# Kernel optimization log

Measured on AMD Instinct MI355X. Metric: run time of the kernel, lower is better.

Reference implementation:

```python
import jax, jax.numpy as jnp
import numpy as np

N_NODES = 50000
N_EDGES = 625000
DIM = 128
DROPOUT_P = 0.5


def setup_inputs() -> dict:
    key = jax.random.key(0)
    kx, ke, kw, kb = jax.random.split(key, 4)
    x = jax.random.normal(kx, (N_NODES, DIM), dtype=jnp.float32)
    edge_index = jax.random.randint(ke, (2, N_EDGES), 0, N_NODES, dtype=jnp.int64)
    # GCNConv linear weight (glorot-ish) and bias
    W = jax.random.normal(kw, (DIM, DIM), dtype=jnp.float32) / np.sqrt(DIM)
    b = jnp.zeros((DIM,), dtype=jnp.float32)
    return {"x": x, "edge_index": edge_index, "W": W, "b": b}


def reference(x, edge_index, W, b):
    N = x.shape[0]
    # --- add self-loops ---
    loop = jnp.arange(N, dtype=edge_index.dtype)
    src = jnp.concatenate([edge_index[0], loop])  # [E+N]
    dst = jnp.concatenate([edge_index[1], loop])  # [E+N]
    # --- symmetric normalization: deg computed on destination nodes ---
    deg = jax.ops.segment_sum(jnp.ones_like(src, dtype=x.dtype), dst, num_segments=N)
    dis = jnp.where(deg > 0, jax.lax.rsqrt(jnp.where(deg > 0, deg, 1.0)), 0.0)
    norm = dis[src] * dis[dst]  # [E+N]
    # --- linear transform, gather, scatter-add ---
    h = x @ W  # [N, D]
    msg = h[src] * norm[:, None]  # [E+N, D]
    out = jax.ops.segment_sum(msg, dst, num_segments=N) + b  # [N, D]
    # --- ReLU + dropout (training mode, fixed key) + residual ---
    out = jax.nn.relu(out)
    keep = jax.random.bernoulli(jax.random.key(42), 1.0 - DROPOUT_P, out.shape)
    out = jnp.where(keep, out / (1.0 - DROPOUT_P), 0.0)
    out = out + x  # residual: input_dim == output_dim
    return out
```

## Files before the change

kernel.cpp:

```cpp
#include <hip/hip_runtime.h>
#include <hip/hip_bf16.h>
#include <stdint.h>

#define NDIM 128
#define LDK 136
#define BSH 9
#define NB_A 1024
#define BCAP 9216

typedef __attribute__((ext_vector_type(8))) short bf16x8;
typedef __attribute__((ext_vector_type(4))) float f32x4;

__device__ __forceinline__ unsigned short f2bf(float f) {
    unsigned u = __float_as_uint(f);
    unsigned r = u + 0x7fffu + ((u >> 16) & 1u);
    return (unsigned short)(r >> 16);
}
__device__ __forceinline__ float bf2f(unsigned short s) {
    return __uint_as_float(((unsigned)s) << 16);
}

__device__ __forceinline__ void load_edge(const unsigned* __restrict__ w, int is64, int E,
                                          int e, int& s, int& d) {
    if (is64) {
        s = (int)w[(size_t)2 * e];
        d = (int)w[(size_t)2 * E + (size_t)2 * e];
    } else {
        s = (int)w[e];
        d = (int)w[(size_t)E + e];
    }
}

__device__ __forceinline__ int detect_is64(const unsigned* __restrict__ w,
                                           int lo, int hi, int t, int* nzflag) {
    if (t == 0) *nzflag = 0;
    __syncthreads();
    int k = lo + t;
    if (k < hi && w[2 * (size_t)k + 1] != 0u) atomicOr(nzflag, 1);
    __syncthreads();
    return *nzflag ? 0 : 1;
}

__global__ __launch_bounds__(256) void hist_kernel(const unsigned* __restrict__ w,
                                                   const float* __restrict__ W,
                                                   unsigned short* __restrict__ WbfT,
                                                   int* __restrict__ hist,
                                                   int* __restrict__ lock,
                                                   int E, int nbuck, int chunk) {
    __shared__ int h[128];
    __shared__ int nzflag;
    int t = threadIdx.x;
    if (t < 128) h[t] = 0;
    if (t == 0 && blockIdx.x == 0) *lock = 0;
    int lo = blockIdx.x * chunk;
    int hi = lo + chunk; if (hi > E) hi = E;
    int is64 = detect_is64(w, lo, hi, t, &nzflag);

    if (blockIdx.x < 64) {
        int idx = blockIdx.x * 256 + t;
        int k = idx >> 7, c = idx & 127;
        WbfT[c * 128 + k] = f2bf(W[idx]);
    }

    for (int e = lo + t; e < hi; e += 256) {
        int s, d; load_edge(w, is64, E, e, s, d);
        atomicAdd(&h[d >> BSH], 1);
    }
    __syncthreads();
    if (t < nbuck) hist[(size_t)t * gridDim.x + blockIdx.x] = h[t];
}

__global__ __launch_bounds__(1024) void scanhist_kernel(int* __restrict__ hist,
                                                        int* __restrict__ btot,
                                                        int* __restrict__ bbase,
                                                        int* __restrict__ off,
                                                        int* __restrict__ lock,
                                                        int NB, int nbuck, int N, int E) {
    __shared__ int s[1024];
    __shared__ int amlast;
    int t = threadIdx.x;
    if (t == 0) amlast = 0;
    size_t base = (size_t)blockIdx.x * NB;
    int v = hist[base + t];
    s[t] = v;
    __syncthreads();
    for (int d = 1; d < 1024; d <<= 1) {
        int add = (t >= d) ? s[t - d] : 0;
        __syncthreads();
        s[t] += add;
        __syncthreads();
    }
    hist[base + t] = s[t] - v;
    if (t == 1023) {
        atomicExch(&btot[blockIdx.x], s[1023]);
        __threadfence();
        int prev = atomicAdd(lock, 1);
        amlast = (prev == nbuck - 1) ? 1 : 0;
    }
    __syncthreads();
    if (amlast) {
        int v2 = (t < nbuck) ? atomicAdd(&btot[t], 0) : 0;
        s[t] = v2;
        __syncthreads();
        for (int d = 1; d < 128; d <<= 1) {
            int add = (t >= d && t < 128) ? s[t - d] : 0;
            __syncthreads();
            if (t < 128) s[t] += add;
            __syncthreads();
        }
        if (t < nbuck) bbase[t] = s[t] - v2;
        if (t == 0) off[N] = E;
    }
}

__global__ __launch_bounds__(256) void bucket_kernel(const unsigned* __restrict__ w,
                                                     const int* __restrict__ hist,
                                                     const int* __restrict__ bbase,
                                                     unsigned* __restrict__ ebuf,
                                                     int E, int nbuck, int chunk) {
    __shared__ int cur[128];
    __shared__ int nzflag;
    int t = threadIdx.x;
    if (t < nbuck) cur[t] = bbase[t] + hist[(size_t)t * gridDim.x + blockIdx.x];
    int lo = blockIdx.x * chunk;
    int hi = lo + chunk; if (hi > E) hi = E;
    int is64 = detect_is64(w, lo, hi, t, &nzflag);
    for (int e = lo + t; e < hi; e += 256) {
        int s, d; load_edge(w, is64, E, e, s, d);
        int b = d >> BSH;
        int p = atomicAdd(&cur[b], 1);
        ebuf[p] = ((unsigned)s << BSH) | (unsigned)(d & 511);
    }
}

__global__ __launch_bounds__(512) void csrgemm_kernel(const unsigned* __restrict__ ebuf,
                                                      const int* __restrict__ bbase,
                                                      const int* __restrict__ btot,
                                                      int* __restrict__ adj,
                                                      int* __restrict__ off,
                                                      float* __restrict__ dis,
                                                      const float* __restrict__ x,
                                                      const unsigned short* __restrict__ WbfT,
                                                      unsigned short* __restrict__ hp,
                                                      int N, int nbuck) {
    __shared__ union {
        struct { int lcnt[512]; int lscan[512]; int cur[512]; int tile[BCAP]; } cs;
        unsigned short Wt[NDIM][LDK];
    } u;
    int t = threadIdx.x;
    if (blockIdx.x < nbuck) {
        int b = blockIdx.x;
        int start = bbase[b], cnt = btot[b];
        u.cs.lcnt[t] = 0;
        __syncthreads();
        for (int i = t; i < cnt; i += 512) atomicAdd(&u.cs.lcnt[ebuf[start + i] & 511], 1);
        __syncthreads();
        int v = u.cs.lcnt[t];
        u.cs.lscan[t] = v;
        __syncthreads();
        for (int d = 1; d < 512; d <<= 1) {
            int add = (t >= d) ? u.cs.lscan[t - d] : 0;
            __syncthreads();
            u.cs.lscan[t] += add;
            __syncthreads();
        }
        int ex = u.cs.lscan[t] - v;
        int node = (b << BSH) + t;
        if (node < N) {
            off[node] = start + ex;
            dis[node] = rsqrtf((float)(v + 1));
        }
        u.cs.cur[t] = ex;
        __syncthreads();
        if (cnt <= BCAP) {
            for (int i = t; i < cnt; i += 512) {
                unsigned wo = ebuf[start + i];
                int p = atomicAdd(&u.cs.cur[wo & 511], 1);
                u.cs.tile[p] = (int)(wo >> BSH);
            }
            __syncthreads();
            for (int i = t; i < cnt; i += 512) adj[start + i] = u.cs.tile[i];
        } else {
            for (int i = t; i < cnt; i += 512) {
                unsigned wo = ebuf[start + i];
                int p = atomicAdd(&u.cs.cur[wo & 511], 1);
                adj[start + p] = (int)(wo >> BSH);
            }
        }
    } else {
        for (int ch = t; ch < 2048; ch += 512) {
            int c = ch >> 4, k8 = (ch & 15) << 3;
            *(bf16x8*)&u.Wt[c][k8] = *(const bf16x8*)(WbfT + c * 128 + k8);
        }
        __syncthreads();
        const int lane = t & 63;
        const int wv = t >> 6;
        const int l15 = lane & 15;
        const int kg = lane >> 4;
        const int rowbase = (blockIdx.x - nbuck) * 128 + wv * 16;
        const int arow = rowbase + l15;

        bf16x8 a[4];
#pragma unroll
        for (int s = 0; s < 4; ++s) {
            bf16x8 tt;
            if (arow < N) {
                const float* p = x + (size_t)arow * NDIM + s * 32 + kg * 8;
                float4 f0 = *(const float4*)p;
                float4 f1 = *(const float4*)(p + 4);
                tt[0] = (short)f2bf(f0.x); tt[1] = (short)f2bf(f0.y);
                tt[2] = (short)f2bf(f0.z); tt[3] = (short)f2bf(f0.w);
                tt[4] = (short)f2bf(f1.x); tt[5] = (short)f2bf(f1.y);
                tt[6] = (short)f2bf(f1.z); tt[7] = (short)f2bf(f1.w);
            } else {
#pragma unroll
                for (int e = 0; e < 8; ++e) tt[e] = 0;
            }
            a[s] = tt;
        }

        f32x4 acc[8];
#pragma unroll
        for (int ct = 0; ct < 8; ++ct) acc[ct] = (f32x4){0.f, 0.f, 0.f, 0.f};
#pragma unroll
        for (int ct = 0; ct < 8; ++ct) {
#pragma unroll
            for (int s = 0; s < 4; ++s) {
                bf16x8 bb = *(const bf16x8*)&u.Wt[ct * 16 + l15][s * 32 + kg * 8];
                acc[ct] = __builtin_amdgcn_mfma_f32_16x16x32_bf16(a[s], bb, acc[ct], 0, 0, 0);
            }
        }

        const int r0 = rowbase + kg * 4;
#pragma unroll
        for (int ct = 0; ct < 8; ++ct) {
            int col = ct * 16 + l15;
#pragma unroll
            for (int j = 0; j < 4; ++j) {
                int r = r0 + j;
                if (r < N) hp[(size_t)r * NDIM + col] = f2bf(acc[ct][j]);
            }
        }
    }
}

__device__ __forceinline__ unsigned rotl32(unsigned v, int d) {
    return (v << d) | (v >> (32 - d));
}
__device__ __forceinline__ unsigned tf_bits(unsigned ctr) {
    unsigned x0 = 0u, x1 = ctr;
    const unsigned ks0 = 0u, ks1 = 42u, ks2 = 0u ^ 42u ^ 0x1BD11BDAu;
    x0 += ks0; x1 += ks1;
#define RND(r) { x0 += x1; x1 = rotl32(x1, (r)); x1 ^= x0; }
    RND(13) RND(15) RND(26) RND(6)   x0 += ks1; x1 += ks2 + 1u;
    RND(17) RND(29) RND(16) RND(24)  x0 += ks2; x1 += ks0 + 2u;
    RND(13) RND(15) RND(26) RND(6)   x0 += ks0; x1 += ks1 + 3u;
    RND(17) RND(29) RND(16) RND(24)  x0 += ks1; x1 += ks2 + 4u;
    RND(13) RND(15) RND(26) RND(6)   x0 += ks2; x1 += ks0 + 5u;
#undef RND
    return x0 ^ x1;
}

__global__ __launch_bounds__(256) void gather_kernel(const unsigned short* __restrict__ hp,
                                                     const float* __restrict__ x,
                                                     const int* __restrict__ off,
                                                     const int* __restrict__ adj,
                                                     const float* __restrict__ dis,
                                                     const float* __restrict__ b,
                                                     float* __restrict__ out, int N) {
    int wid = (int)((blockIdx.x * 256u + threadIdx.x) >> 6);
    int lane = threadIdx.x & 63;
    int half = lane >> 5;
    int l32 = lane & 31;
    int node = wid * 2 + half;
    bool valid = node < N;
    int nodec = valid ? node : N - 1;
    const float dn = dis[nodec];
    const int c0 = l32 * 4;
    const unsigned short* hpc = hp + c0;

    unsigned ctr = (unsigned)(nodec * NDIM + c0);
    unsigned bt0 = tf_bits(ctr);
    unsigned bt1 = tf_bits(ctr + 1u);
    unsigned bt2 = tf_bits(ctr + 2u);
    unsigned bt3 = tf_bits(ctr + 3u);

    uint2 hv = *(const uint2*)(hpc + (size_t)nodec * NDIM);
    float a00 = bf2f((unsigned short)hv.x) * dn, a01 = bf2f((unsigned short)(hv.x >> 16)) * dn;
    float a02 = bf2f((unsigned short)hv.y) * dn, a03 = bf2f((unsigned short)(hv.y >> 16)) * dn;
    float a10 = 0.f, a11 = 0.f, a12 = 0.f, a13 = 0.f;
    float a20 = 0.f, a21 = 0.f, a22 = 0.f, a23 = 0.f;
    float a30 = 0.f, a31 = 0.f, a32 = 0.f, a33 = 0.f;

    int k0 = valid ? off[nodec] : 0;
    int k1 = valid ? off[nodec + 1] : 0;
    int kb = k0;
    const int sbase = half << 5;
    while (kb < k1) {
        int nb = k1 - kb; if (nb > 32) nb = 32;
        int myadj = (kb + l32 < k1) ? adj[kb + l32] : 0;
        float mydis = dis[myadj];
        int j = 0;
        for (; j + 8 <= nb; j += 8) {
            int s0 = __shfl(myadj, sbase + j);
            int s1 = __shfl(myadj, sbase + j + 1);
            int s2 = __shfl(myadj, sbase + j + 2);
            int s3 = __shfl(myadj, sbase + j + 3);
            int s4 = __shfl(myadj, sbase + j + 4);
            int s5 = __shfl(myadj, sbase + j + 5);
            int s6 = __shfl(myadj, sbase + j + 6);
            int s7 = __shfl(myadj, sbase + j + 7);
            uint2 v0 = *(const uint2*)(hpc + (size_t)s0 * NDIM);
            uint2 v1 = *(const uint2*)(hpc + (size_t)s1 * NDIM);
            uint2 v2 = *(const uint2*)(hpc + (size_t)s2 * NDIM);
            uint2 v3 = *(const uint2*)(hpc + (size_t)s3 * NDIM);
            uint2 v4 = *(const uint2*)(hpc + (size_t)s4 * NDIM);
            uint2 v5 = *(const uint2*)(hpc + (size_t)s5 * NDIM);
            uint2 v6 = *(const uint2*)(hpc + (size_t)s6 * NDIM);
            uint2 v7 = *(const uint2*)(hpc + (size_t)s7 * NDIM);
            float n0 = __shfl(mydis, sbase + j);
            float n1 = __shfl(mydis, sbase + j + 1);
            float n2 = __shfl(mydis, sbase + j + 2);
            float n3 = __shfl(mydis, sbase + j + 3);
            float n4 = __shfl(mydis, sbase + j + 4);
            float n5 = __shfl(mydis, sbase + j + 5);
            float n6 = __shfl(mydis, sbase + j + 6);
            float n7 = __shfl(mydis, sbase + j + 7);
            a00 = fmaf(bf2f((unsigned short)v0.x), n0, a00);
            a01 = fmaf(bf2f((unsigned short)(v0.x >> 16)), n0, a01);
            a02 = fmaf(bf2f((unsigned short)v0.y), n0, a02);
            a03 = fmaf(bf2f((unsigned short)(v0.y >> 16)), n0, a03);
            a10 = fmaf(bf2f((unsigned short)v1.x), n1, a10);
            a11 = fmaf(bf2f((unsigned short)(v1.x >> 16)), n1, a11);
            a12 = fmaf(bf2f((unsigned short)v1.y), n1, a12);
            a13 = fmaf(bf2f((unsigned short)(v1.y >> 16)), n1, a13);
            a20 = fmaf(bf2f((unsigned short)v2.x), n2, a20);
            a21 = fmaf(bf2f((unsigned short)(v2.x >> 16)), n2, a21);
            a22 = fmaf(bf2f((unsigned short)v2.y), n2, a22);
            a23 = fmaf(bf2f((unsigned short)(v2.y >> 16)), n2, a23);
            a30 = fmaf(bf2f((unsigned short)v3.x), n3, a30);
            a31 = fmaf(bf2f((unsigned short)(v3.x >> 16)), n3, a31);
            a32 = fmaf(bf2f((unsigned short)v3.y), n3, a32);
            a33 = fmaf(bf2f((unsigned short)(v3.y >> 16)), n3, a33);
            a00 = fmaf(bf2f((unsigned short)v4.x), n4, a00);
            a01 = fmaf(bf2f((unsigned short)(v4.x >> 16)), n4, a01);
            a02 = fmaf(bf2f((unsigned short)v4.y), n4, a02);
            a03 = fmaf(bf2f((unsigned short)(v4.y >> 16)), n4, a03);
            a10 = fmaf(bf2f((unsigned short)v5.x), n5, a10);
            a11 = fmaf(bf2f((unsigned short)(v5.x >> 16)), n5, a11);
            a12 = fmaf(bf2f((unsigned short)v5.y), n5, a12);
            a13 = fmaf(bf2f((unsigned short)(v5.y >> 16)), n5, a13);
            a20 = fmaf(bf2f((unsigned short)v6.x), n6, a20);
            a21 = fmaf(bf2f((unsigned short)(v6.x >> 16)), n6, a21);
            a22 = fmaf(bf2f((unsigned short)v6.y), n6, a22);
            a23 = fmaf(bf2f((unsigned short)(v6.y >> 16)), n6, a23);
            a30 = fmaf(bf2f((unsigned short)v7.x), n7, a30);
            a31 = fmaf(bf2f((unsigned short)(v7.x >> 16)), n7, a31);
            a32 = fmaf(bf2f((unsigned short)v7.y), n7, a32);
            a33 = fmaf(bf2f((unsigned short)(v7.y >> 16)), n7, a33);
        }
        for (; j < nb; ++j) {
            int s = __shfl(myadj, sbase + j);
            float nn = __shfl(mydis, sbase + j);
            uint2 v = *(const uint2*)(hpc + (size_t)s * NDIM);
            a00 = fmaf(bf2f((unsigned short)v.x), nn, a00);
            a01 = fmaf(bf2f((unsigned short)(v.x >> 16)), nn, a01);
            a02 = fmaf(bf2f((unsigned short)v.y), nn, a02);
            a03 = fmaf(bf2f((unsigned short)(v.y >> 16)), nn, a03);
        }
        kb += nb;
    }

    float c0s = (a00 + a10) + (a20 + a30);
    float c1s = (a01 + a11) + (a21 + a31);
    float c2s = (a02 + a12) + (a22 + a32);
    float c3s = (a03 + a13) + (a23 + a33);

    float4 bb = *(const float4*)(b + c0);
    float v0 = fmaxf(fmaf(dn, c0s, bb.x), 0.f);
    float v1 = fmaxf(fmaf(dn, c1s, bb.y), 0.f);
    float v2 = fmaxf(fmaf(dn, c2s, bb.z), 0.f);
    float v3 = fmaxf(fmaf(dn, c3s, bb.w), 0.f);

    v0 = (bt0 >> 31) ? 0.f : v0 * 2.f;
    v1 = (bt1 >> 31) ? 0.f : v1 * 2.f;
    v2 = (bt2 >> 31) ? 0.f : v2 * 2.f;
    v3 = (bt3 >> 31) ? 0.f : v3 * 2.f;

    if (valid) {
        float4 xr = *(const float4*)(x + (size_t)node * NDIM + c0);
        float4 o;
        o.x = v0 + xr.x; o.y = v1 + xr.y; o.z = v2 + xr.z; o.w = v3 + xr.w;
        *(float4*)(out + (size_t)node * NDIM + c0) = o;
    }
}

extern "C" void kernel_launch(void* const* d_in, const int* in_sizes, int n_in,
                              void* d_out, int out_size, void* d_ws, size_t ws_size,
                              hipStream_t stream) {
    const float* x = (const float*)d_in[0];
    const unsigned* edge_w = (const unsigned*)d_in[1];
    const float* W = (const float*)d_in[2];
    const float* b = (const float*)d_in[3];
    float* out = (float*)d_out;

    const int N = in_sizes[0] / NDIM;
    const int E = in_sizes[1] / 2;
    const int nbuck = (N + (1 << BSH) - 1) >> BSH;
    const int chunk = (E + NB_A - 1) / NB_A;
    const int ntiles = (N + 127) / 128;

    char* ws = (char*)d_ws;
    unsigned short* hp = (unsigned short*)ws;
    float* dis   = (float*)(ws + (size_t)N * NDIM * sizeof(short));
    int*   off   = (int*)((char*)dis + (size_t)N * sizeof(float));
    int*   adj   = (int*)((char*)off + (size_t)(N + 4) * sizeof(int));
    unsigned* ebuf = (unsigned*)((char*)adj + (size_t)E * sizeof(int));
    int*   hist  = (int*)((char*)ebuf + (size_t)E * sizeof(unsigned));
    int*   btot  = (int*)((char*)hist + (size_t)128 * NB_A * sizeof(int));
    int*   bbase = (int*)((char*)btot + (size_t)128 * sizeof(int));
    int*   lock  = (int*)((char*)bbase + (size_t)128 * sizeof(int));
    unsigned short* WbfT = (unsigned short*)((char*)lock + 64);

    hist_kernel<<<NB_A, 256, 0, stream>>>(edge_w, W, WbfT, hist, lock, E, nbuck, chunk);
    scanhist_kernel<<<nbuck, 1024, 0, stream>>>(hist, btot, bbase, off, lock, NB_A, nbuck, N, E);
    bucket_kernel<<<NB_A, 256, 0, stream>>>(edge_w, hist, bbase, ebuf, E, nbuck, chunk);
    csrgemm_kernel<<<nbuck + ntiles, 512, 0, stream>>>(ebuf, bbase, btot, adj, off, dis,
                                                       x, WbfT, hp, N, nbuck);

    int waves = (N + 1) / 2;
    gather_kernel<<<(waves + 3) / 4, 256, 0, stream>>>(hp, x, off, adj, dis, b, out, N);
}
```

Measured before the change: 74.02 us.

## Replace histogram+scan bucketing with fixed-capacity buckets and atomic reservation

Removes the separate per-block histogram pass and the cross-block scan kernel. Each block now counts its edges per bucket locally, reserves space with one global atomic per bucket, and writes into a fixed-capacity slot per bucket. The CSR kernel rebuilds bucket offsets with a small in-block scan. This saves one full read of the edge list and a kernel launch. In exchange it relies on no bucket exceeding 8192 edges (about 6.4k expected here), and the adjacency order within a bucket is no longer deterministic.

```diff
diff --git a/kernel.cpp b/kernel.cpp
--- a/kernel.cpp
+++ b/kernel.cpp
@@ -6,6 +6,7 @@
 #define LDK 136
 #define BSH 9
 #define NB_A 1024
+#define BCAPG 8192
 #define BCAP 9216
 
 typedef __attribute__((ext_vector_type(8))) short bf16x8;
@@ -41,101 +42,48 @@
     return *nzflag ? 0 : 1;
 }
 
-__global__ __launch_bounds__(256) void hist_kernel(const unsigned* __restrict__ w,
-                                                   const float* __restrict__ W,
+__global__ __launch_bounds__(256) void prep_kernel(const float* __restrict__ W,
                                                    unsigned short* __restrict__ WbfT,
-                                                   int* __restrict__ hist,
-                                                   int* __restrict__ lock,
-                                                   int E, int nbuck, int chunk) {
-    __shared__ int h[128];
+                                                   int* __restrict__ cur_g) {
+    int t = threadIdx.x;
+    int idx = blockIdx.x * 256 + t;
+    int k = idx >> 7, c = idx & 127;
+    WbfT[c * 128 + k] = f2bf(W[idx]);
+    if (blockIdx.x == 0 && t < 128) cur_g[t] = 0;
+}
+
+__global__ __launch_bounds__(256) void bucket_kernel(const unsigned* __restrict__ w,
+                                                     int* __restrict__ cur_g,
+                                                     unsigned* __restrict__ ebuf,
+                                                     int E, int nbuck, int chunk) {
+    __shared__ int lcur[128];
     __shared__ int nzflag;
     int t = threadIdx.x;
-    if (t < 128) h[t] = 0;
-    if (t == 0 && blockIdx.x == 0) *lock = 0;
+    if (t < 128) lcur[t] = 0;
     int lo = blockIdx.x * chunk;
     int hi = lo + chunk; if (hi > E) hi = E;
     int is64 = detect_is64(w, lo, hi, t, &nzflag);
 
-    if (blockIdx.x < 64) {
-        int idx = blockIdx.x * 256 + t;
-        int k = idx >> 7, c = idx & 127;
-        WbfT[c * 128 + k] = f2bf(W[idx]);
-    }
-
     for (int e = lo + t; e < hi; e += 256) {
         int s, d; load_edge(w, is64, E, e, s, d);
-        atomicAdd(&h[d >> BSH], 1);
+        atomicAdd(&lcur[d >> BSH], 1);
     }
     __syncthreads();
-    if (t < nbuck) hist[(size_t)t * gridDim.x + blockIdx.x] = h[t];
-}
-
-__global__ __launch_bounds__(1024) void scanhist_kernel(int* __restrict__ hist,
-                                                        int* __restrict__ btot,
-                                                        int* __restrict__ bbase,
-                                                        int* __restrict__ off,
-                                                        int* __restrict__ lock,
-                                                        int NB, int nbuck, int N, int E) {
-    __shared__ int s[1024];
-    __shared__ int amlast;
-    int t = threadIdx.x;
-    if (t == 0) amlast = 0;
-    size_t base = (size_t)blockIdx.x * NB;
-    int v = hist[base + t];
-    s[t] = v;
+    if (t < nbuck) {
+        int c = lcur[t];
+        lcur[t] = (c > 0) ? atomicAdd(&cur_g[t], c) : 0;
+    }
     __syncthreads();
-    for (int d = 1; d < 1024; d <<= 1) {
-        int add = (t >= d) ? s[t - d] : 0;
-        __syncthreads();
-        s[t] += add;
-        __syncthreads();
-    }
-    hist[base + t] = s[t] - v;
-    if (t == 1023) {
-        atomicExch(&btot[blockIdx.x], s[1023]);
-        __threadfence();
-        int prev = atomicAdd(lock, 1);
-        amlast = (prev == nbuck - 1) ? 1 : 0;
-    }
-    __syncthreads();
-    if (amlast) {
-        int v2 = (t < nbuck) ? atomicAdd(&btot[t], 0) : 0;
-        s[t] = v2;
-        __syncthreads();
-        for (int d = 1; d < 128; d <<= 1) {
-            int add = (t >= d && t < 128) ? s[t - d] : 0;
-            __syncthreads();
-            if (t < 128) s[t] += add;
-            __syncthreads();
-        }
-        if (t < nbuck) bbase[t] = s[t] - v2;
-        if (t == 0) off[N] = E;
-    }
-}
-
-__global__ __launch_bounds__(256) void bucket_kernel(const unsigned* __restrict__ w,
-                                                     const int* __restrict__ hist,
-                                                     const int* __restrict__ bbase,
-                                                     unsigned* __restrict__ ebuf,
-                                                     int E, int nbuck, int chunk) {
-    __shared__ int cur[128];
-    __shared__ int nzflag;
-    int t = threadIdx.x;
-    if (t < nbuck) cur[t] = bbase[t] + hist[(size_t)t * gridDim.x + blockIdx.x];
-    int lo = blockIdx.x * chunk;
-    int hi = lo + chunk; if (hi > E) hi = E;
-    int is64 = detect_is64(w, lo, hi, t, &nzflag);
     for (int e = lo + t; e < hi; e += 256) {
         int s, d; load_edge(w, is64, E, e, s, d);
         int b = d >> BSH;
-        int p = atomicAdd(&cur[b], 1);
-        ebuf[p] = ((unsigned)s << BSH) | (unsigned)(d & 511);
+        int p = atomicAdd(&lcur[b], 1);
+        ebuf[(size_t)b * BCAPG + p] = ((unsigned)s << BSH) | (unsigned)(d & 511);
     }
 }
 
 __global__ __launch_bounds__(512) void csrgemm_kernel(const unsigned* __restrict__ ebuf,
-                                                      const int* __restrict__ bbase,
-                                                      const int* __restrict__ btot,
+                                                      const int* __restrict__ cur_g,
                                                       int* __restrict__ adj,
                                                       int* __restrict__ off,
                                                       float* __restrict__ dis,
@@ -144,16 +92,28 @@
                                                       unsigned short* __restrict__ hp,
                                                       int N, int nbuck) {
     __shared__ union {
-        struct { int lcnt[512]; int lscan[512]; int cur[512]; int tile[BCAP]; } cs;
+        struct { int lcnt[512]; int lscan[512]; int cur[512]; int bsc[128]; int tile[BCAP]; } cs;
         unsigned short Wt[NDIM][LDK];
     } u;
     int t = threadIdx.x;
     if (blockIdx.x < nbuck) {
         int b = blockIdx.x;
-        int start = bbase[b], cnt = btot[b];
+        if (t < 128) u.cs.bsc[t] = (t < nbuck) ? cur_g[t] : 0;
+        __syncthreads();
+        for (int d = 1; d < 128; d <<= 1) {
+            int add = (t >= d && t < 128) ? u.cs.bsc[t - d] : 0;
+            __syncthreads();
+            if (t < 128) u.cs.bsc[t] += add;
+            __syncthreads();
+        }
+        int cnt = cur_g[b];
+        int start = u.cs.bsc[b] - cnt;
+        if (b == 0 && t == 0) off[N] = u.cs.bsc[127];
+        const unsigned* ebase = ebuf + (size_t)b * BCAPG;
+
         u.cs.lcnt[t] = 0;
         __syncthreads();
-        for (int i = t; i < cnt; i += 512) atomicAdd(&u.cs.lcnt[ebuf[start + i] & 511], 1);
+        for (int i = t; i < cnt; i += 512) atomicAdd(&u.cs.lcnt[ebase[i] & 511], 1);
         __syncthreads();
         int v = u.cs.lcnt[t];
         u.cs.lscan[t] = v;
@@ -174,7 +134,7 @@
         __syncthreads();
         if (cnt <= BCAP) {
             for (int i = t; i < cnt; i += 512) {
-                unsigned wo = ebuf[start + i];
+                unsigned wo = ebase[i];
                 int p = atomicAdd(&u.cs.cur[wo & 511], 1);
                 u.cs.tile[p] = (int)(wo >> BSH);
             }
@@ -182,7 +142,7 @@
             for (int i = t; i < cnt; i += 512) adj[start + i] = u.cs.tile[i];
         } else {
             for (int i = t; i < cnt; i += 512) {
-                unsigned wo = ebuf[start + i];
+                unsigned wo = ebase[i];
                 int p = atomicAdd(&u.cs.cur[wo & 511], 1);
                 adj[start + p] = (int)(wo >> BSH);
             }
@@ -416,16 +376,12 @@
     int*   off   = (int*)((char*)dis + (size_t)N * sizeof(float));
     int*   adj   = (int*)((char*)off + (size_t)(N + 4) * sizeof(int));
     unsigned* ebuf = (unsigned*)((char*)adj + (size_t)E * sizeof(int));
-    int*   hist  = (int*)((char*)ebuf + (size_t)E * sizeof(unsigned));
-    int*   btot  = (int*)((char*)hist + (size_t)128 * NB_A * sizeof(int));
-    int*   bbase = (int*)((char*)btot + (size_t)128 * sizeof(int));
-    int*   lock  = (int*)((char*)bbase + (size_t)128 * sizeof(int));
-    unsigned short* WbfT = (unsigned short*)((char*)lock + 64);
-
-    hist_kernel<<<NB_A, 256, 0, stream>>>(edge_w, W, WbfT, hist, lock, E, nbuck, chunk);
-    scanhist_kernel<<<nbuck, 1024, 0, stream>>>(hist, btot, bbase, off, lock, NB_A, nbuck, N, E);
-    bucket_kernel<<<NB_A, 256, 0, stream>>>(edge_w, hist, bbase, ebuf, E, nbuck, chunk);
-    csrgemm_kernel<<<nbuck + ntiles, 512, 0, stream>>>(ebuf, bbase, btot, adj, off, dis,
+    int*   cur_g = (int*)((char*)ebuf + (size_t)128 * BCAPG * sizeof(unsigned));
+    unsigned short* WbfT = (unsigned short*)((char*)cur_g + 128 * sizeof(int));
+
+    prep_kernel<<<64, 256, 0, stream>>>(W, WbfT, cur_g);
+    bucket_kernel<<<NB_A, 256, 0, stream>>>(edge_w, cur_g, ebuf, E, nbuck, chunk);
+    csrgemm_kernel<<<nbuck + ntiles, 512, 0, stream>>>(ebuf, cur_g, adj, off, dis,
                                                        x, WbfT, hp, N, nbuck);
 
     int waves = (N + 1) / 2;
```

After: 91.51 us. +23.6%, slower.
